# Kernel tuning notes

Measured on AMD Instinct MI355X. Metric: run time of the kernel, lower is better.

Reference implementation:

```python
import jax, jax.numpy as jnp
import numpy as np

TAU = 0.8
V_TH = 0.5
W_D1_GPI = -0.8
W_D2_STN = 0.5
W_STN_GPI = 0.6
GPI_TONIC = 0.4
NOISE = 0.1
T, B = 512, 256
N_D1, N_D2, N_GPI, N_STN = 128, 128, 64, 64


def setup_inputs() -> dict:
    key = jax.random.key(0)
    ks = jax.random.split(key, 7)
    return {
        "x": jax.random.normal(ks[0], (T, B, 2), dtype=jnp.float32),
        "dopa": jax.random.uniform(ks[1], (T, B), dtype=jnp.float32),
        "rpe": jax.random.normal(ks[2], (T, B), dtype=jnp.float32),
        "W_d1": jax.random.normal(ks[3], (N_D1, 2), dtype=jnp.float32) * 0.5,
        "W_d2": jax.random.normal(ks[4], (N_D2, 2), dtype=jnp.float32) * 0.5,
        "noise_d1": jax.random.normal(ks[5], (T, B, N_D1), dtype=jnp.float32),
        "noise_d2": jax.random.normal(ks[6], (T, B, N_D2), dtype=jnp.float32),
    }


def reference(x, dopa, rpe, W_d1, W_d2, noise_d1, noise_d2):
    """Runs T LIF steps of the spiking basal-ganglia circuit for B circuits.

    Returns gates [T, B] = d1_rate - gpi_rate per step. rpe is unused (as in source).
    """
    dt = x.dtype
    v0 = (
        jnp.zeros((B, N_D1), dt),
        jnp.zeros((B, N_D2), dt),
        jnp.zeros((B, N_GPI), dt),
        jnp.zeros((B, N_STN), dt),
    )

    def lif(v, I):
        v = TAU * v + (1.0 - TAU) * I
        s = (v >= V_TH).astype(dt)
        return v * (1.0 - s), s

    def step(carry, inp):
        v_d1, v_d2, v_gpi, v_stn = carry
        xt, dop, nd1, nd2 = inp  # [B,2], [B], [B,N], [B,N]
        d1_mod = (1.0 + dop * 0.5)[:, None]
        d2_mod = (1.0 - dop * 0.3)[:, None]
        I_d1 = jnp.einsum("bi,ni->bn", xt, W_d1) * d1_mod
        v_d1, s_d1 = lif(v_d1, I_d1 + nd1 * NOISE)
        I_d2 = jnp.einsum("bi,ni->bn", xt, W_d2) * d2_mod
        v_d2, s_d2 = lif(v_d2, I_d2 + nd2 * NOISE)
        I_stn = (s_d2.mean(axis=1) * W_D2_STN)[:, None]  # [B,1] broadcast to [B,N_STN]
        v_stn, s_stn = lif(v_stn, I_stn)
        I_gpi = (GPI_TONIC + s_d1.mean(axis=1) * W_D1_GPI + s_stn.mean(axis=1) * W_STN_GPI)[:, None]
        v_gpi, s_gpi = lif(v_gpi, I_gpi)
        gate = s_d1.mean(axis=1) - s_gpi.mean(axis=1)  # [B]
        return (v_d1, v_d2, v_gpi, v_stn), gate

    _, gates = jax.lax.scan(step, v0, (x, dopa, noise_d1, noise_d2))
    return gates  # [T, B]
```

## Files before the change

### kernel.cpp

```cpp
#include <hip/hip_runtime.h>


__global__ __launch_bounds__(256, 1) void bg_kernel(
    const float* __restrict__ x,
    const float* __restrict__ dopa,
    const float* __restrict__ Wd1,
    const float* __restrict__ Wd2,
    const float* __restrict__ nd1,
    const float* __restrict__ nd2,
    float* __restrict__ out)
{
#pragma clang fp contract(off)
    constexpr int T = 512, B = 256;
    constexpr size_t TSTRIDE = (size_t)B * 128;

    __shared__ float lds_xm[T][4];
    __shared__ uint4 cnt_lds[T];

    const int b    = blockIdx.x;
    const int tid  = threadIdx.x;
    const int wv   = tid >> 6;
    const int lane = tid & 63;
    const int pop  = wv >> 1;
    const int half = wv & 1;

    for (int t = tid; t < T; t += 256) {
        const float2 xv = *(const float2*)(x + (size_t)t * (B * 2) + b * 2);
        const float dop = dopa[(size_t)t * B + b];
        lds_xm[t][0] = xv.x;
        lds_xm[t][1] = xv.y;
        lds_xm[t][2] = 1.0f + dop * 0.5f;
        lds_xm[t][3] = 1.0f - dop * 0.3f;
    }
    __syncthreads();

    {
        const int n = half * 64 + lane;
        const float* nb = (pop ? nd2 : nd1) + (size_t)b * 128 + n;
        const float2 w  = *(const float2*)((pop ? Wd2 : Wd1) + 2 * n);

        float va = 0.0f;
        unsigned int cnt_reg = 0u;

        float arrA[16], arrB[16];

#define LOADG(dst, t0)                                                       \
        { _Pragma("unroll")                                                  \
          for (int k = 0; k < 16; ++k)                                       \
              dst[k] = nb[(size_t)((t0) + k) * TSTRIDE]; }

#define PROCG(src, t0, lbase)                                                \
        { _Pragma("unroll")                                                  \
          for (int k = 0; k < 16; ++k) {                                     \
              const float4 xm = *(const float4*)&lds_xm[(t0) + k][0];        \
              const float m   = pop ? xm.w : xm.z;                           \
              const float dot = __builtin_fmaf(xm.y, w.y, xm.x * w.x);       \
              const float I   = dot * m + src[k] * 0.1f;                     \
              va = 0.8f * va + 0.2f * I;                                     \
              const bool s = va >= 0.5f;                                     \
              va = s ? 0.0f : va;                                            \
              const int c = __popcll(__ballot(s));                           \
              cnt_reg = (lane == (lbase) + k) ? (unsigned int)c : cnt_reg;   \
          } }

        LOADG(arrA, 0)
        LOADG(arrB, 16)
        for (int gp = 0; gp < 16; ++gp) {
            const int t0 = gp * 32;
            const int lb = (gp & 1) * 32;
            PROCG(arrA, t0, lb)
            if (gp < 15) LOADG(arrA, t0 + 32)
            PROCG(arrB, t0 + 16, lb + 16)
            if (gp < 15) LOADG(arrB, t0 + 48)
            if (gp & 1) {
                const int tw = (gp - 1) * 32;
                ((unsigned int*)&cnt_lds[tw + lane])[wv] = cnt_reg;
            }
        }
#undef LOADG
#undef PROCG
    }

    __syncthreads();

    if (wv == 0) {
        float v_stn = 0.0f, v_gpi = 0.0f;

        for (int g = 0; g < 8; ++g) {
            const uint4 c4 = cnt_lds[g * 64 + lane];
            const float mean1v = (float)(int)(c4.x + c4.y) * 0.0078125f;
            const float mean2v = (float)(int)(c4.z + c4.w) * 0.0078125f;

            float gate_reg = 0.0f;
#pragma unroll
            for (int j = 0; j < 64; ++j) {
                const float mean1 = __shfl(mean1v, j);
                const float mean2 = __shfl(mean2v, j);

                const float I_stn = mean2 * 0.5f;
                v_stn = 0.8f * v_stn + 0.2f * I_stn;
                const float s_stn = (v_stn >= 0.5f) ? 1.0f : 0.0f;
                v_stn = (v_stn >= 0.5f) ? 0.0f : v_stn;

                const float I_gpi = (0.4f + mean1 * -0.8f) + s_stn * 0.6f;
                v_gpi = 0.8f * v_gpi + 0.2f * I_gpi;
                const float s_gpi = (v_gpi >= 0.5f) ? 1.0f : 0.0f;
                v_gpi = (v_gpi >= 0.5f) ? 0.0f : v_gpi;

                const float gate = mean1 - s_gpi;

                gate_reg = (lane == j) ? gate : gate_reg;
            }
            out[(size_t)(g * 64 + lane) * B + b] = gate_reg;
        }
    }
}

extern "C" void kernel_launch(void* const* d_in, const int* in_sizes, int n_in,
                              void* d_out, int out_size, void* d_ws, size_t ws_size,
                              hipStream_t stream) {
    const float* x    = (const float*)d_in[0];
    const float* dopa = (const float*)d_in[1];
    const float* Wd1  = (const float*)d_in[3];
    const float* Wd2  = (const float*)d_in[4];
    const float* nd1  = (const float*)d_in[5];
    const float* nd2  = (const float*)d_in[6];
    float* out = (float*)d_out;

    bg_kernel<<<dim3(256), dim3(256), 0, stream>>>(x, dopa, Wd1, Wd2, nd1, nd2, out);
}
```

Before: 186.8 us.

## Split into per-population wave kernel and separate batched STN/GPi scan kernel

Phase 1 now uses one 64-lane wave per (population, pair of batch circuits), with each lane handling four neurons through float4 noise loads. Spike counts are packed as bytes and written into the output buffer as scratch, and the block index is remapped across XCDs. A second tiny kernel then runs the sequential STN/GPi recurrence with one thread per circuit, replacing the serial shuffle loop that previously ran in a single wave per block. This removes the idle waves in the old block's tail phase and widens memory accesses, at the cost of an extra launch and byte-granular global stores.

Measured after the change: 242.9 us. 1.3x slower.

```diff
diff --git a/kernel.cpp b/kernel.cpp
--- a/kernel.cpp
+++ b/kernel.cpp
@@ -1,7 +1,7 @@
 #include <hip/hip_runtime.h>
 
 
-__global__ __launch_bounds__(256, 1) void bg_kernel(
+__global__ __launch_bounds__(64, 1) void bg_phase1(
     const float* __restrict__ x,
     const float* __restrict__ dopa,
     const float* __restrict__ Wd1,
@@ -14,106 +14,145 @@
     constexpr int T = 512, B = 256;
     constexpr size_t TSTRIDE = (size_t)B * 128;
 
-    __shared__ float lds_xm[T][4];
-    __shared__ uint4 cnt_lds[T];
+    __shared__ float lds_xm[T][2][4];
 
-    const int b    = blockIdx.x;
-    const int tid  = threadIdx.x;
-    const int wv   = tid >> 6;
-    const int lane = tid & 63;
-    const int pop  = wv >> 1;
-    const int half = wv & 1;
+    const int beta = blockIdx.x;
+    const int lane = threadIdx.x;
+    const int xcd  = beta & 7;
+    const int slot = beta >> 3;
+    const int a    = slot & 1;
+    const int p    = xcd * 16 + (slot >> 1);
+    const int b0   = 2 * p;
 
-    for (int t = tid; t < T; t += 256) {
-        const float2 xv = *(const float2*)(x + (size_t)t * (B * 2) + b * 2);
-        const float dop = dopa[(size_t)t * B + b];
-        lds_xm[t][0] = xv.x;
-        lds_xm[t][1] = xv.y;
-        lds_xm[t][2] = 1.0f + dop * 0.5f;
-        lds_xm[t][3] = 1.0f - dop * 0.3f;
+    for (int t = lane; t < T; t += 64) {
+        const float4 xv = *(const float4*)(x + (size_t)t * (B * 2) + b0 * 2);
+        const float2 dv = *(const float2*)(dopa + (size_t)t * B + b0);
+        lds_xm[t][0][0] = xv.x;  lds_xm[t][0][1] = xv.y;
+        lds_xm[t][0][2] = 1.0f + dv.x * 0.5f;
+        lds_xm[t][0][3] = 1.0f - dv.x * 0.3f;
+        lds_xm[t][1][0] = xv.z;  lds_xm[t][1][1] = xv.w;
+        lds_xm[t][1][2] = 1.0f + dv.y * 0.5f;
+        lds_xm[t][1][3] = 1.0f - dv.y * 0.3f;
     }
     __syncthreads();
 
-    {
-        const int n = half * 64 + lane;
-        const float* nb = (pop ? nd2 : nd1) + (size_t)b * 128 + n;
-        const float2 w  = *(const float2*)((pop ? Wd2 : Wd1) + 2 * n);
+    const float* na = (a ? nd2 : nd1) + (size_t)b0 * 128 + 4 * lane;
+    const float* Wa = a ? Wd2 : Wd1;
+    const int cL  = lane >> 5;
+    const int nb4 = 4 * (lane & 31);
+    const float4 W01 = *(const float4*)(Wa + 2 * nb4);
+    const float4 W23 = *(const float4*)(Wa + 2 * nb4 + 4);
 
-        float va = 0.0f;
-        unsigned int cnt_reg = 0u;
+    float v0 = 0.0f, v1 = 0.0f, v2 = 0.0f, v3 = 0.0f;
+    unsigned int cnt_reg = 0u;
 
-        float arrA[16], arrB[16];
+    float4 arrA[16], arrB[16];
 
 #define LOADG(dst, t0)                                                       \
-        { _Pragma("unroll")                                                  \
-          for (int k = 0; k < 16; ++k)                                       \
-              dst[k] = nb[(size_t)((t0) + k) * TSTRIDE]; }
+    { _Pragma("unroll")                                                      \
+      for (int k = 0; k < 16; ++k)                                           \
+          dst[k] = *(const float4*)(na + (size_t)((t0) + k) * TSTRIDE); }
 
 #define PROCG(src, t0, lbase)                                                \
-        { _Pragma("unroll")                                                  \
-          for (int k = 0; k < 16; ++k) {                                     \
-              const float4 xm = *(const float4*)&lds_xm[(t0) + k][0];        \
-              const float m   = pop ? xm.w : xm.z;                           \
-              const float dot = __builtin_fmaf(xm.y, w.y, xm.x * w.x);       \
-              const float I   = dot * m + src[k] * 0.1f;                     \
-              va = 0.8f * va + 0.2f * I;                                     \
-              const bool s = va >= 0.5f;                                     \
-              va = s ? 0.0f : va;                                            \
-              const int c = __popcll(__ballot(s));                           \
-              cnt_reg = (lane == (lbase) + k) ? (unsigned int)c : cnt_reg;   \
-          } }
+    { _Pragma("unroll")                                                      \
+      for (int k = 0; k < 16; ++k) {                                         \
+          const float4 xm = *(const float4*)&lds_xm[(t0) + k][cL][0];        \
+          const float m = a ? xm.w : xm.z;                                   \
+          const float d0 = __builtin_fmaf(xm.y, W01.y, xm.x * W01.x);        \
+          const float I0 = d0 * m + src[k].x * 0.1f;                         \
+          v0 = 0.8f * v0 + 0.2f * I0;                                        \
+          const bool s0 = v0 >= 0.5f; v0 = s0 ? 0.0f : v0;                   \
+          const float d1 = __builtin_fmaf(xm.y, W01.w, xm.x * W01.z);        \
+          const float I1 = d1 * m + src[k].y * 0.1f;                         \
+          v1 = 0.8f * v1 + 0.2f * I1;                                        \
+          const bool s1 = v1 >= 0.5f; v1 = s1 ? 0.0f : v1;                   \
+          const float d2 = __builtin_fmaf(xm.y, W23.y, xm.x * W23.x);        \
+          const float I2 = d2 * m + src[k].z * 0.1f;                         \
+          v2 = 0.8f * v2 + 0.2f * I2;                                        \
+          const bool s2 = v2 >= 0.5f; v2 = s2 ? 0.0f : v2;                   \
+          const float d3 = __builtin_fmaf(xm.y, W23.w, xm.x * W23.z);        \
+          const float I3 = d3 * m + src[k].w * 0.1f;                         \
+          v3 = 0.8f * v3 + 0.2f * I3;                                        \
+          const bool s3 = v3 >= 0.5f; v3 = s3 ? 0.0f : v3;                   \
+          const unsigned long long m0 = __ballot(s0);                        \
+          const unsigned long long m1b = __ballot(s1);                       \
+          const unsigned long long m2b = __ballot(s2);                       \
+          const unsigned long long m3b = __ballot(s3);                       \
+          const unsigned int cA = (unsigned int)(                            \
+              __popcll(m0 & 0xFFFFFFFFull) + __popcll(m1b & 0xFFFFFFFFull) + \
+              __popcll(m2b & 0xFFFFFFFFull) + __popcll(m3b & 0xFFFFFFFFull));\
+          const unsigned int cB = (unsigned int)(                            \
+              __popcll(m0 >> 32) + __popcll(m1b >> 32) +                     \
+              __popcll(m2b >> 32) + __popcll(m3b >> 32));                    \
+          const unsigned int pk = cA | (cB << 8);                            \
+          cnt_reg = (lane == (lbase) + k) ? pk : cnt_reg;                    \
+      } }
 
-        LOADG(arrA, 0)
-        LOADG(arrB, 16)
-        for (int gp = 0; gp < 16; ++gp) {
-            const int t0 = gp * 32;
-            const int lb = (gp & 1) * 32;
-            PROCG(arrA, t0, lb)
-            if (gp < 15) LOADG(arrA, t0 + 32)
-            PROCG(arrB, t0 + 16, lb + 16)
-            if (gp < 15) LOADG(arrB, t0 + 48)
-            if (gp & 1) {
-                const int tw = (gp - 1) * 32;
-                ((unsigned int*)&cnt_lds[tw + lane])[wv] = cnt_reg;
-            }
+    LOADG(arrA, 0)
+    LOADG(arrB, 16)
+    for (int gp = 0; gp < 16; ++gp) {
+        const int t0 = gp * 32;
+        const int lb = (gp & 1) * 32;
+        PROCG(arrA, t0, lb)
+        if (gp < 15) LOADG(arrA, t0 + 32)
+        PROCG(arrB, t0 + 16, lb + 16)
+        if (gp < 15) LOADG(arrB, t0 + 48)
+        if (gp & 1) {
+            const int tw = (gp - 1) * 32;
+            unsigned char* ob =
+                (unsigned char*)(out + (size_t)(tw + lane) * B + b0) + 2 * a;
+            ob[0] = (unsigned char)(cnt_reg & 0xFFu);
+            ob[4] = (unsigned char)((cnt_reg >> 8) & 0xFFu);
         }
+    }
 #undef LOADG
 #undef PROCG
+}
+
+__global__ __launch_bounds__(64, 1) void bg_phase2(
+    float* __restrict__ out)
+{
+#pragma clang fp contract(off)
+    constexpr int T = 512, B = 256;
+    const int b = blockIdx.x * 64 + threadIdx.x;
+    const unsigned int* ib = (const unsigned int*)out + b;
+
+    float v_stn = 0.0f, v_gpi = 0.0f;
+    unsigned int A2[8], B2[8];
+
+#define LOADG2(dst, t0)                                                      \
+    { _Pragma("unroll")                                                      \
+      for (int k = 0; k < 8; ++k) dst[k] = ib[(size_t)((t0) + k) * B]; }
+
+#define PROCG2(src, t0)                                                      \
+    { _Pragma("unroll")                                                      \
+      for (int k = 0; k < 8; ++k) {                                          \
+          const int c1 = (int)(src[k] & 0xFFu);                              \
+          const int c2 = (int)((src[k] >> 16) & 0xFFu);                      \
+          const float mean1 = (float)c1 * 0.0078125f;                        \
+          const float mean2 = (float)c2 * 0.0078125f;                        \
+          const float I_stn = mean2 * 0.5f;                                  \
+          v_stn = 0.8f * v_stn + 0.2f * I_stn;                               \
+          const float s_stn = (v_stn >= 0.5f) ? 1.0f : 0.0f;                 \
+          v_stn = (v_stn >= 0.5f) ? 0.0f : v_stn;                            \
+          const float I_gpi = (0.4f + mean1 * -0.8f) + s_stn * 0.6f;         \
+          v_gpi = 0.8f * v_gpi + 0.2f * I_gpi;                               \
+          const float s_gpi = (v_gpi >= 0.5f) ? 1.0f : 0.0f;                 \
+          v_gpi = (v_gpi >= 0.5f) ? 0.0f : v_gpi;                            \
+          out[(size_t)((t0) + k) * B + b] = mean1 - s_gpi;                   \
+      } }
+
+    LOADG2(A2, 0)
+    LOADG2(B2, 8)
+    for (int g = 0; g < 32; ++g) {
+        const int t0 = g * 16;
+        PROCG2(A2, t0)
+        if (g < 31) LOADG2(A2, t0 + 16)
+        PROCG2(B2, t0 + 8)
+        if (g < 31) LOADG2(B2, t0 + 24)
     }
-
-    __syncthreads();
-
-    if (wv == 0) {
-        float v_stn = 0.0f, v_gpi = 0.0f;
-
-        for (int g = 0; g < 8; ++g) {
-            const uint4 c4 = cnt_lds[g * 64 + lane];
-            const float mean1v = (float)(int)(c4.x + c4.y) * 0.0078125f;
-            const float mean2v = (float)(int)(c4.z + c4.w) * 0.0078125f;
-
-            float gate_reg = 0.0f;
-#pragma unroll
-            for (int j = 0; j < 64; ++j) {
-                const float mean1 = __shfl(mean1v, j);
-                const float mean2 = __shfl(mean2v, j);
-
-                const float I_stn = mean2 * 0.5f;
-                v_stn = 0.8f * v_stn + 0.2f * I_stn;
-                const float s_stn = (v_stn >= 0.5f) ? 1.0f : 0.0f;
-                v_stn = (v_stn >= 0.5f) ? 0.0f : v_stn;
-
-                const float I_gpi = (0.4f + mean1 * -0.8f) + s_stn * 0.6f;
-                v_gpi = 0.8f * v_gpi + 0.2f * I_gpi;
-                const float s_gpi = (v_gpi >= 0.5f) ? 1.0f : 0.0f;
-                v_gpi = (v_gpi >= 0.5f) ? 0.0f : v_gpi;
-
-                const float gate = mean1 - s_gpi;
-
-                gate_reg = (lane == j) ? gate : gate_reg;
-            }
-            out[(size_t)(g * 64 + lane) * B + b] = gate_reg;
-        }
-    }
+#undef LOADG2
+#undef PROCG2
 }
 
 extern "C" void kernel_launch(void* const* d_in, const int* in_sizes, int n_in,
@@ -127,5 +166,6 @@
     const float* nd2  = (const float*)d_in[6];
     float* out = (float*)d_out;
 
-    bg_kernel<<<dim3(256), dim3(256), 0, stream>>>(x, dopa, Wd1, Wd2, nd1, nd2, out);
+    bg_phase1<<<dim3(256), dim3(64), 0, stream>>>(x, dopa, Wd1, Wd2, nd1, nd2, out);
+    bg_phase2<<<dim3(4), dim3(64), 0, stream>>>(out);
 }
```
